# Optimization experiments

Hardware: AMD Instinct MI355X
Metric: run time of the kernel (lower is better)

Reference implementation:

```python
import jax, jax.numpy as jnp
import numpy as np

N = 50000
E = 1600000
DIM = 128
RC = 5.0
DEPTH = 3


def setup_inputs() -> dict:
    key = jax.random.key(0)
    kv, ke, ks, kd, kw, kb, krs, ksig = jax.random.split(key, 8)
    v = jax.random.normal(kv, (N, DIM), dtype=jnp.float32)
    # edge distances in [0, rc]
    e = jax.random.uniform(ke, (E, 1), dtype=jnp.float32) * RC
    src = jax.random.randint(ks, (E,), 0, N, dtype=jnp.int32)
    dst = jax.random.randint(kd, (E,), 0, N, dtype=jnp.int32)
    # learned params: A = nn.Linear(dim, dim); rs, sigma = torch.rand(1)
    A_w = jax.random.normal(kw, (DIM, DIM), dtype=jnp.float32) / np.sqrt(DIM)
    A_b = jax.random.normal(kb, (DIM,), dtype=jnp.float32) * 0.01
    rs = jax.random.uniform(krs, (1,), dtype=jnp.float32)
    sigma = jax.random.uniform(ksig, (1,), dtype=jnp.float32)
    return {"v": v, "e": e, "src": src, "dst": dst,
            "A_w": A_w, "A_b": A_b, "rs": rs, "sigma": sigma}


def _edge_envelope(r, rs, sigma):
    # exp(-(r-rs)^2/sigma^2) * 0.5 * cos(pi*r/rc) * (r < rc)
    gauss = jnp.exp(-jnp.square(r - rs) / jnp.square(sigma))
    cutoff = 0.5 * jnp.cos(np.pi * r / RC) * (r < RC).astype(r.dtype)
    return gauss * cutoff


def reference(v, e, src, dst, A_w, A_b, rs, sigma):
    f = _edge_envelope(e, rs, sigma)  # [E, 1]
    cur = v
    for _ in range(DEPTH):
        msg = f * cur[src]  # gather src node feats, weight by edge envelope: [E, DIM]
        svf = jax.ops.segment_sum(msg, dst, num_segments=N)  # scatter-sum to dst: [N, DIM]
        cur = jax.nn.relu((svf + v) @ A_w.T + A_b)  # linear + relu, skip from original v
    return cur
```

## Files before the change

### kernel.cpp

```cpp
#include <hip/hip_runtime.h>
#include <math.h>

#define N_NODES 50000
#define N_PAD   50048
#define N_EDGES 1600000
#define DIM     128
#define RCUT    5.0f
#define NGROUP  (N_PAD / 64)
#define NB_PRE  512
#define CH_PRE  (N_EDGES / NB_PRE)
#define NB_CONV 6250
#define NB_WPREP 8
#define NB_SUB  8
#define B_SUB   (NB_PRE / NB_SUB)
#define XPAD    136
#define NTILE   (N_PAD / 16)
#define NB_MID  32

typedef __attribute__((ext_vector_type(8))) __bf16 bf16x8;
typedef __attribute__((ext_vector_type(4))) float  f32x4;

__device__ __forceinline__ float bf_lo(unsigned int u) { return __uint_as_float(u << 16); }
__device__ __forceinline__ float bf_hi(unsigned int u) { return __uint_as_float(u & 0xffff0000u); }
__device__ __forceinline__ unsigned short f2bf(float x) {
    unsigned int u = __float_as_uint(x);
    u += 0x7fffu + ((u >> 16) & 1u);
    return (unsigned short)(u >> 16);
}

__global__ __launch_bounds__(256) void preA_kernel(
        const float* __restrict__ v, unsigned short* __restrict__ vb,
        const float* __restrict__ Aw, uint4* __restrict__ wfrag,
        const int* __restrict__ dst, int* __restrict__ partial,
        int* __restrict__ bar) {
    int b = blockIdx.x;
    if (b < NB_CONV) {
        int i = b * 256 + threadIdx.x;
        float4 x = ((const float4*)v)[i];
        uint2 o;
        o.x = (unsigned)f2bf(x.x) | ((unsigned)f2bf(x.y) << 16);
        o.y = (unsigned)f2bf(x.z) | ((unsigned)f2bf(x.w) << 16);
        ((uint2*)vb)[i] = o;
    } else if (b < NB_CONV + NB_WPREP) {
        int t = (b - NB_CONV) * 256 + threadIdx.x;
        if (b == NB_CONV && threadIdx.x <= NB_MID)
            bar[threadIdx.x * 32] = 0;
        int lane = t & 63, nt = (t >> 6) & 7, kk = t >> 9;
        int n  = nt * 16 + (lane & 15);
        int k0 = kk * 32 + (lane >> 4) * 8;
        unsigned short h[8];
        #pragma unroll
        for (int i = 0; i < 8; ++i) h[i] = f2bf(Aw[n * DIM + k0 + i]);
        uint4 o;
        o.x = h[0] | ((unsigned)h[1] << 16); o.y = h[2] | ((unsigned)h[3] << 16);
        o.z = h[4] | ((unsigned)h[5] << 16); o.w = h[6] | ((unsigned)h[7] << 16);
        wfrag[t] = o;
    } else {
        __shared__ int h[NGROUP];
        int cb = b - NB_CONV - NB_WPREP, tid = threadIdx.x;
        for (int g = tid; g < NGROUP; g += 256) h[g] = 0;
        __syncthreads();
        int beg = cb * CH_PRE, end = beg + CH_PRE;
        for (int i = beg + tid; i < end; i += 256)
            atomicAdd(&h[dst[i] >> 6], 1);
        __syncthreads();
        for (int g = tid; g < NGROUP; g += 256) partial[cb * NGROUP + g] = h[g];
    }
}

__device__ __forceinline__ void gsync32(int* bar) {
    int* rel = bar + NB_MID * 32;
    __syncthreads();
    if (threadIdx.x == 0) {
        __threadfence();
        __hip_atomic_store(&bar[blockIdx.x * 32], 1,
                           __ATOMIC_RELAXED, __HIP_MEMORY_SCOPE_AGENT);
    }
    if (blockIdx.x == 0) {
        if (threadIdx.x < NB_MID) {
            int* cp = &bar[threadIdx.x * 32];
            while (__hip_atomic_load(cp, __ATOMIC_RELAXED,
                                     __HIP_MEMORY_SCOPE_AGENT) == 0)
                __builtin_amdgcn_s_sleep(1);
        }
        __syncthreads();
        if (threadIdx.x == 0) {
            __threadfence();
            __hip_atomic_store(rel, 1, __ATOMIC_RELAXED, __HIP_MEMORY_SCOPE_AGENT);
        }
    }
    if (threadIdx.x == 0) {
        while (__hip_atomic_load(rel, __ATOMIC_RELAXED,
                                 __HIP_MEMORY_SCOPE_AGENT) == 0)
            __builtin_amdgcn_s_sleep(1);
        __threadfence();
    }
    __syncthreads();
}

__global__ __launch_bounds__(256) void kmid_kernel(
        const int* __restrict__ partial,
        int* __restrict__ partial2,
        int* __restrict__ goff,
        int* __restrict__ pbase,
        int* __restrict__ bar) {
    __shared__ int part[256];
    __shared__ int goffL[NGROUP];
    int tid = threadIdx.x, bid = blockIdx.x;
    int gb = bid & 3, bb = bid >> 2;
    int g = gb * 256 + tid;

    if (g < NGROUP) {
        int s = 0;
        int b0 = bb * B_SUB;
        for (int b = b0; b < b0 + B_SUB; ++b) s += partial[b * NGROUP + g];
        partial2[bb * NGROUP + g] = s;
    }
    gsync32(bar);

    int i0 = tid * 4;
    int v[4]; int s = 0;
    #pragma unroll
    for (int k = 0; k < 4; ++k) {
        int i = i0 + k; int t = 0;
        if (i < NGROUP) {
            #pragma unroll
            for (int b2 = 0; b2 < NB_SUB; ++b2) t += partial2[b2 * NGROUP + i];
        }
        v[k] = t; s += t;
    }
    part[tid] = s; __syncthreads();
    for (int d = 1; d < 256; d <<= 1) {
        int val = (tid >= d) ? part[tid - d] : 0;
        __syncthreads(); part[tid] += val; __syncthreads();
    }
    int run = (tid == 0) ? 0 : part[tid - 1];
    #pragma unroll
    for (int k = 0; k < 4; ++k) {
        int i = i0 + k;
        if (i < NGROUP) {
            goffL[i] = run;
            if (bid == 0) goff[i] = run;
            run += v[k];
        }
    }
    if (bid == 0 && tid == 0) goff[NGROUP] = N_EDGES;
    __syncthreads();

    if (g < NGROUP) {
        int r = goffL[g];
        for (int b2 = 0; b2 < bb; ++b2) r += partial2[b2 * NGROUP + g];
        int b0 = bb * B_SUB;
        for (int b = b0; b < b0 + B_SUB; ++b) {
            pbase[b * NGROUP + g] = r;
            r += partial[b * NGROUP + g];
        }
    }
}

__global__ __launch_bounds__(512) void reorder_kernel(
        const float* __restrict__ e,
        const int*   __restrict__ src,
        const int*   __restrict__ dst,
        const float* __restrict__ rs,
        const float* __restrict__ sigma,
        const int*   __restrict__ pbase,
        int2* __restrict__ metaT) {
    __shared__ int base[NGROUP];
    __shared__ int cnt[NGROUP];
    int b = blockIdx.x, tid = threadIdx.x;
    for (int g = tid; g < NGROUP; g += 512) { base[g] = pbase[b * NGROUP + g]; cnt[g] = 0; }
    __syncthreads();
    float rsv = rs[0], sg = sigma[0];
    int beg = b * CH_PRE, end = beg + CH_PRE;
    for (int i = beg + tid; i < end; i += 512) {
        float r  = e[i];
        float d  = r - rsv;
        float gauss = expf(-(d * d) / (sg * sg));
        float cut   = 0.5f * cosf(r * (float)(M_PI / (double)RCUT));
        cut = (r < RCUT) ? cut : 0.0f;
        float fe = gauss * cut;
        int dn = dst[i];
        int g  = dn >> 6;
        int lr = atomicAdd(&cnt[g], 1);
        metaT[base[g] + lr] = make_int2(src[i] * (DIM * 2) | ((dn & 63) << 24),
                                        __float_as_int(fe));
    }
}

#define EDGE2(mx, mf, rr)                                        \
    do {                                                         \
        float ff = __int_as_float(mf);                           \
        a0 = fmaf(ff, bf_lo(rr), a0);                            \
        a1 = fmaf(ff, bf_hi(rr), a1);                            \
    } while (0)

__device__ __forceinline__ void gather_node(
        const int2* __restrict__ meta, const char* basec,
        int beg, int end, float& a0, float& a1) {
    int c = beg;
    if ((c & 1) && c < end) {
        int2 m = meta[c];
        unsigned rr = *(const unsigned*)(basec + (unsigned)m.x);
        EDGE2(m.x, m.y, rr);
        ++c;
    }
    for (; c + 16 <= end; c += 16) {
        int4 m0 = *(const int4*)(meta + c);
        int4 m1 = *(const int4*)(meta + c + 2);
        int4 m2 = *(const int4*)(meta + c + 4);
        int4 m3 = *(const int4*)(meta + c + 6);
        int4 m4 = *(const int4*)(meta + c + 8);
        int4 m5 = *(const int4*)(meta + c + 10);
        int4 m6 = *(const int4*)(meta + c + 12);
        int4 m7 = *(const int4*)(meta + c + 14);
        unsigned r0  = *(const unsigned*)(basec + (unsigned)m0.x);
        unsigned r1  = *(const unsigned*)(basec + (unsigned)m0.z);
        unsigned r2  = *(const unsigned*)(basec + (unsigned)m1.x);
        unsigned r3  = *(const unsigned*)(basec + (unsigned)m1.z);
        unsigned r4  = *(const unsigned*)(basec + (unsigned)m2.x);
        unsigned r5  = *(const unsigned*)(basec + (unsigned)m2.z);
        unsigned r6  = *(const unsigned*)(basec + (unsigned)m3.x);
        unsigned r7  = *(const unsigned*)(basec + (unsigned)m3.z);
        unsigned r8  = *(const unsigned*)(basec + (unsigned)m4.x);
        unsigned r9  = *(const unsigned*)(basec + (unsigned)m4.z);
        unsigned r10 = *(const unsigned*)(basec + (unsigned)m5.x);
        unsigned r11 = *(const unsigned*)(basec + (unsigned)m5.z);
        unsigned r12 = *(const unsigned*)(basec + (unsigned)m6.x);
        unsigned r13 = *(const unsigned*)(basec + (unsigned)m6.z);
        unsigned r14 = *(const unsigned*)(basec + (unsigned)m7.x);
        unsigned r15 = *(const unsigned*)(basec + (unsigned)m7.z);
        EDGE2(m0.x, m0.y, r0);  EDGE2(m0.z, m0.w, r1);
        EDGE2(m1.x, m1.y, r2);  EDGE2(m1.z, m1.w, r3);
        EDGE2(m2.x, m2.y, r4);  EDGE2(m2.z, m2.w, r5);
        EDGE2(m3.x, m3.y, r6);  EDGE2(m3.z, m3.w, r7);
        EDGE2(m4.x, m4.y, r8);  EDGE2(m4.z, m4.w, r9);
        EDGE2(m5.x, m5.y, r10); EDGE2(m5.z, m5.w, r11);
        EDGE2(m6.x, m6.y, r12); EDGE2(m6.z, m6.w, r13);
        EDGE2(m7.x, m7.y, r14); EDGE2(m7.z, m7.w, r15);
    }
    if (c + 8 <= end) {
        int4 m0 = *(const int4*)(meta + c);
        int4 m1 = *(const int4*)(meta + c + 2);
        int4 m2 = *(const int4*)(meta + c + 4);
        int4 m3 = *(const int4*)(meta + c + 6);
        unsigned r0 = *(const unsigned*)(basec + (unsigned)m0.x);
        unsigned r1 = *(const unsigned*)(basec + (unsigned)m0.z);
        unsigned r2 = *(const unsigned*)(basec + (unsigned)m1.x);
        unsigned r3 = *(const unsigned*)(basec + (unsigned)m1.z);
        unsigned r4 = *(const unsigned*)(basec + (unsigned)m2.x);
        unsigned r5 = *(const unsigned*)(basec + (unsigned)m2.z);
        unsigned r6 = *(const unsigned*)(basec + (unsigned)m3.x);
        unsigned r7 = *(const unsigned*)(basec + (unsigned)m3.z);
        EDGE2(m0.x, m0.y, r0); EDGE2(m0.z, m0.w, r1);
        EDGE2(m1.x, m1.y, r2); EDGE2(m1.z, m1.w, r3);
        EDGE2(m2.x, m2.y, r4); EDGE2(m2.z, m2.w, r5);
        EDGE2(m3.x, m3.y, r6); EDGE2(m3.z, m3.w, r7);
        c += 8;
    }
    for (; c < end; ++c) {
        int2 m = meta[c];
        unsigned rr = *(const unsigned*)(basec + (unsigned)m.x);
        EDGE2(m.x, m.y, rr);
    }
}

__global__ __launch_bounds__(512) void layer0_kernel(
        const unsigned short* __restrict__ cur,
        const unsigned short* __restrict__ vb,
        const int2*  __restrict__ metaT,
        const int*   __restrict__ goff,
        int2* __restrict__ meta,
        int*  __restrict__ off,
        const uint4* __restrict__ wfrag,
        const float* __restrict__ bias,
        unsigned short* __restrict__ out_bf) {
    __shared__ unsigned short xlds[64 * XPAD];
    __shared__ int c64[64], b64[65], cu64[64];
    int tid = threadIdx.x;
    int wv  = tid >> 6, lane = tid & 63;
    int g   = blockIdx.x;
    int sbeg = goff[g], send = goff[g + 1];

    if (tid < 64) c64[tid] = 0;
    __syncthreads();
    for (int i = sbeg + tid; i < send; i += 512)
        atomicAdd(&c64[(metaT[i].x >> 24) & 63], 1);
    __syncthreads();
    if (tid == 0) {
        int run = 0;
        #pragma unroll
        for (int t = 0; t < 64; ++t) { b64[t] = run; cu64[t] = run; run += c64[t]; }
        b64[64] = run;
    }
    __syncthreads();
    if (tid < 64) {
        int node = g * 64 + tid;
        if (node <= N_NODES) off[node] = sbeg + b64[tid];
    }
    for (int i = sbeg + tid; i < send; i += 512) {
        int2 m = metaT[i];
        int tag = (m.x >> 24) & 63;
        int lr = atomicAdd(&cu64[tag], 1);
        meta[sbeg + lr] = make_int2(m.x & 0x00FFFFFF, m.y);
    }
    __syncthreads();

    int n0 = g * 64 + wv * 8;
    int myoff = 0;
    if (lane < 9) myoff = sbeg + b64[wv * 8 + lane];
    const char* basec = (const char*)cur + lane * 4;

    #pragma unroll 1
    for (int q = 0; q < 8; ++q) {
        int nl = wv * 8 + q;
        int n  = n0 + q;
        float a0 = 0.f, a1 = 0.f;
        if (n < N_NODES) {
            unsigned vv = *(const unsigned*)((const char*)vb + (size_t)n * (DIM * 2) + lane * 4);
            a0 = bf_lo(vv); a1 = bf_hi(vv);
            int beg = __builtin_amdgcn_readlane(myoff, q);
            int end = __builtin_amdgcn_readlane(myoff, q + 1);
            gather_node(meta, basec, beg, end, a0, a1);
        }
        *(unsigned*)(xlds + nl * XPAD + lane * 2) =
            (unsigned)f2bf(a0) | ((unsigned)f2bf(a1) << 16);
    }
    __syncthreads();

    int quad = lane >> 4, l16 = lane & 15;
    int rb = wv >> 1, nh = wv & 1;
    f32x4 acc[4];
    #pragma unroll
    for (int j = 0; j < 4; ++j) acc[j] = (f32x4){0.f, 0.f, 0.f, 0.f};

    const unsigned short* xp = xlds + (rb * 16 + l16) * XPAD + quad * 8;
    #pragma unroll
    for (int kk = 0; kk < 4; ++kk) {
        bf16x8 af = *(const bf16x8*)(xp + kk * 32);
        #pragma unroll
        for (int j = 0; j < 4; ++j) {
            uint4 w = wfrag[(kk * 8 + nh * 4 + j) * 64 + lane];
            bf16x8 bfr = __builtin_bit_cast(bf16x8, w);
            acc[j] = __builtin_amdgcn_mfma_f32_16x16x32_bf16(af, bfr, acc[j], 0, 0, 0);
        }
    }

    int orow0 = g * 64 + rb * 16 + quad * 4;
    #pragma unroll
    for (int j = 0; j < 4; ++j) {
        int col = (nh * 4 + j) * 16 + l16;
        float b = bias[col];
        #pragma unroll
        for (int r = 0; r < 4; ++r) {
            int orow = orow0 + r;
            if (orow < N_NODES)
                out_bf[(size_t)orow * DIM + col] = f2bf(fmaxf(acc[j][r] + b, 0.f));
        }
    }
}

__global__ __launch_bounds__(128, 8) void layer12_kernel(
        const unsigned short* __restrict__ cur,
        const unsigned short* __restrict__ vb,
        const int2*  __restrict__ meta,
        const int*   __restrict__ off,
        const uint4* __restrict__ wfrag,
        const float* __restrict__ bias,
        unsigned short* __restrict__ out_bf,
        float* __restrict__ out_f,
        int last) {
    __shared__ unsigned short xlds[16 * XPAD];
    int tid = threadIdx.x;
    int wv  = tid >> 6, lane = tid & 63;
    int tile = blockIdx.x;
    int n0  = tile * 16 + wv * 8;

    int offidx = n0 + ((lane < 9) ? lane : 8);
    if (offidx > N_NODES) offidx = N_NODES;
    int myoff = off[offidx];
    const char* basec = (const char*)cur + lane * 4;

    #pragma unroll 1
    for (int q = 0; q < 8; ++q) {
        int nl = wv * 8 + q;
        int n  = n0 + q;
        float a0 = 0.f, a1 = 0.f;
        if (n < N_NODES) {
            unsigned vv = *(const unsigned*)((const char*)vb + (size_t)n * (DIM * 2) + lane * 4);
            a0 = bf_lo(vv); a1 = bf_hi(vv);
            int beg = __builtin_amdgcn_readlane(myoff, q);
            int end = __builtin_amdgcn_readlane(myoff, q + 1);
            gather_node(meta, basec, beg, end, a0, a1);
        }
        *(unsigned*)(xlds + nl * XPAD + lane * 2) =
            (unsigned)f2bf(a0) | ((unsigned)f2bf(a1) << 16);
    }
    __syncthreads();

    int quad = lane >> 4, l16 = lane & 15;
    f32x4 acc[4];
    #pragma unroll
    for (int j = 0; j < 4; ++j) acc[j] = (f32x4){0.f, 0.f, 0.f, 0.f};

    const unsigned short* xp = xlds + l16 * XPAD + quad * 8;
    #pragma unroll
    for (int kk = 0; kk < 4; ++kk) {
        bf16x8 af = *(const bf16x8*)(xp + kk * 32);
        #pragma unroll
        for (int j = 0; j < 4; ++j) {
            uint4 w = wfrag[(kk * 8 + wv * 4 + j) * 64 + lane];
            bf16x8 bfr = __builtin_bit_cast(bf16x8, w);
            acc[j] = __builtin_amdgcn_mfma_f32_16x16x32_bf16(af, bfr, acc[j], 0, 0, 0);
        }
    }

    int orow0 = tile * 16 + quad * 4;
    #pragma unroll
    for (int j = 0; j < 4; ++j) {
        int col = (wv * 4 + j) * 16 + l16;
        float b = bias[col];
        #pragma unroll
        for (int r = 0; r < 4; ++r) {
            int orow = orow0 + r;
            if (orow < N_NODES) {
                float val = fmaxf(acc[j][r] + b, 0.f);
                if (last) out_f[(size_t)orow * DIM + col] = val;
                else      out_bf[(size_t)orow * DIM + col] = f2bf(val);
            }
        }
    }
}

extern "C" void kernel_launch(void* const* d_in, const int* in_sizes, int n_in,
                              void* d_out, int out_size, void* d_ws, size_t ws_size,
                              hipStream_t stream) {
    const float* v     = (const float*)d_in[0];
    const float* e     = (const float*)d_in[1];
    const int*   src   = (const int*)  d_in[2];
    const int*   dst   = (const int*)  d_in[3];
    const float* Aw    = (const float*)d_in[4];
    const float* Ab    = (const float*)d_in[5];
    const float* rs    = (const float*)d_in[6];
    const float* sigma = (const float*)d_in[7];
    float* out = (float*)d_out;

    char* p = (char*)d_ws;
    int2*           meta  = (int2*)p;            p += (size_t)N_EDGES * 8;
    unsigned short* bufV  = (unsigned short*)p;  p += (size_t)N_PAD * DIM * 2;
    unsigned short* bufA  = (unsigned short*)p;  p += (size_t)N_PAD * DIM * 2;
    unsigned short* bufB  = (unsigned short*)p;  p += (size_t)N_PAD * DIM * 2;
    uint4*          wfrag = (uint4*)p;           p += 2048 * 16;
    int*            off   = (int*)p;             p += (size_t)(N_NODES + 2) * 4;
    int*            goff  = (int*)p;             p += (NGROUP + 2) * 4;
    int*            bar   = (int*)p;             p += (NB_MID + 1) * 32 * 4;
    int2* metaT    = (int2*)bufA;
    int*  partial  = (int*)bufB;
    int*  pbase    = partial + NB_PRE * NGROUP;
    int*  partial2 = pbase + NB_PRE * NGROUP;

    preA_kernel<<<NB_CONV + NB_WPREP + NB_PRE, 256, 0, stream>>>(
        v, bufV, Aw, wfrag, dst, partial, bar);
    kmid_kernel<<<NB_MID, 256, 0, stream>>>(partial, partial2, goff, pbase, bar);
    reorder_kernel<<<NB_PRE, 512, 0, stream>>>(e, src, dst, rs, sigma, pbase, metaT);

    layer0_kernel<<<NGROUP, 512, 0, stream>>>(
        bufV, bufV, metaT, goff, meta, off, wfrag, Ab, bufB);
    layer12_kernel<<<NTILE, 128, 0, stream>>>(
        bufB, bufV, meta, off, wfrag, Ab, bufA, nullptr, 0);
    layer12_kernel<<<NTILE, 128, 0, stream>>>(
        bufA, bufV, meta, off, wfrag, Ab, nullptr, out, 1);
}
```

Baseline: 318.3 us.

## Bucket edges by 16-node groups and shrink layer0 blocks to 16-node tiles

Changes the counting-sort granularity from 64-node groups to 16-node groups, so the histogram, prefix scan and reorder all work on 3128 buckets. The reorder runs on 128 blocks that each cover four histogram chunks. layer0 now processes one 16-node tile per 128-thread block, matching layer12. This is meant to raise parallelism and occupancy in layer0 and shorten its per-block local sort. In exchange, the mid scan kernel needs more blocks in its grid-wide sync, and the reorder has fewer, larger blocks.

Result: slower. 348.7 us (+9.6%).

```diff
diff --git a/kernel.cpp b/kernel.cpp
--- a/kernel.cpp
+++ b/kernel.cpp
@@ -6,16 +6,16 @@
 #define N_EDGES 1600000
 #define DIM     128
 #define RCUT    5.0f
-#define NGROUP  (N_PAD / 64)
+#define NG16    (N_PAD / 16)
 #define NB_PRE  512
 #define CH_PRE  (N_EDGES / NB_PRE)
 #define NB_CONV 6250
 #define NB_WPREP 8
-#define NB_SUB  8
-#define B_SUB   (NB_PRE / NB_SUB)
+#define NB_RE   128
+#define CH_RE   (N_EDGES / NB_RE)
 #define XPAD    136
-#define NTILE   (N_PAD / 16)
-#define NB_MID  32
+#define NB_MID  104
+#define GCHK    13
 
 typedef __attribute__((ext_vector_type(8))) __bf16 bf16x8;
 typedef __attribute__((ext_vector_type(4))) float  f32x4;
@@ -56,19 +56,19 @@
         o.z = h[4] | ((unsigned)h[5] << 16); o.w = h[6] | ((unsigned)h[7] << 16);
         wfrag[t] = o;
     } else {
-        __shared__ int h[NGROUP];
+        __shared__ int h[NG16];
         int cb = b - NB_CONV - NB_WPREP, tid = threadIdx.x;
-        for (int g = tid; g < NGROUP; g += 256) h[g] = 0;
+        for (int g = tid; g < NG16; g += 256) h[g] = 0;
         __syncthreads();
         int beg = cb * CH_PRE, end = beg + CH_PRE;
         for (int i = beg + tid; i < end; i += 256)
-            atomicAdd(&h[dst[i] >> 6], 1);
+            atomicAdd(&h[dst[i] >> 4], 1);
         __syncthreads();
-        for (int g = tid; g < NGROUP; g += 256) partial[cb * NGROUP + g] = h[g];
-    }
-}
-
-__device__ __forceinline__ void gsync32(int* bar) {
+        for (int g = tid; g < NG16; g += 256) partial[cb * NG16 + g] = h[g];
+    }
+}
+
+__device__ __forceinline__ void gsyncm(int* bar) {
     int* rel = bar + NB_MID * 32;
     __syncthreads();
     if (threadIdx.x == 0) {
@@ -105,29 +105,29 @@
         int* __restrict__ pbase,
         int* __restrict__ bar) {
     __shared__ int part[256];
-    __shared__ int goffL[NGROUP];
+    __shared__ int goffL[NG16];
     int tid = threadIdx.x, bid = blockIdx.x;
-    int gb = bid & 3, bb = bid >> 2;
+    int gb = bid % 13, bb = bid / 13;
     int g = gb * 256 + tid;
 
-    if (g < NGROUP) {
+    if (g < NG16) {
         int s = 0;
-        int b0 = bb * B_SUB;
-        for (int b = b0; b < b0 + B_SUB; ++b) s += partial[b * NGROUP + g];
-        partial2[bb * NGROUP + g] = s;
-    }
-    gsync32(bar);
-
-    int i0 = tid * 4;
-    int v[4]; int s = 0;
-    #pragma unroll
-    for (int k = 0; k < 4; ++k) {
+        int b0 = bb * 64;
+        for (int b = b0; b < b0 + 64; ++b) s += partial[b * NG16 + g];
+        partial2[bb * NG16 + g] = s;
+    }
+    gsyncm(bar);
+
+    int i0 = tid * GCHK;
+    int vv[GCHK]; int s = 0;
+    #pragma unroll
+    for (int k = 0; k < GCHK; ++k) {
         int i = i0 + k; int t = 0;
-        if (i < NGROUP) {
+        if (i < NG16) {
             #pragma unroll
-            for (int b2 = 0; b2 < NB_SUB; ++b2) t += partial2[b2 * NGROUP + i];
-        }
-        v[k] = t; s += t;
+            for (int b2 = 0; b2 < 8; ++b2) t += partial2[b2 * NG16 + i];
+        }
+        vv[k] = t; s += t;
     }
     part[tid] = s; __syncthreads();
     for (int d = 1; d < 256; d <<= 1) {
@@ -136,24 +136,26 @@
     }
     int run = (tid == 0) ? 0 : part[tid - 1];
     #pragma unroll
-    for (int k = 0; k < 4; ++k) {
+    for (int k = 0; k < GCHK; ++k) {
         int i = i0 + k;
-        if (i < NGROUP) {
+        if (i < NG16) {
             goffL[i] = run;
             if (bid == 0) goff[i] = run;
-            run += v[k];
-        }
-    }
-    if (bid == 0 && tid == 0) goff[NGROUP] = N_EDGES;
-    __syncthreads();
-
-    if (g < NGROUP) {
+            run += vv[k];
+        }
+    }
+    if (bid == 0 && tid == 0) goff[NG16] = N_EDGES;
+    __syncthreads();
+
+    if (g < NG16) {
         int r = goffL[g];
-        for (int b2 = 0; b2 < bb; ++b2) r += partial2[b2 * NGROUP + g];
-        int b0 = bb * B_SUB;
-        for (int b = b0; b < b0 + B_SUB; ++b) {
-            pbase[b * NGROUP + g] = r;
-            r += partial[b * NGROUP + g];
+        for (int b2 = 0; b2 < bb; ++b2) r += partial2[b2 * NG16 + g];
+        #pragma unroll 1
+        for (int j = 0; j < 16; ++j) {
+            int rc = bb * 16 + j;
+            pbase[rc * NG16 + g] = r;
+            #pragma unroll
+            for (int c = 0; c < 4; ++c) r += partial[(rc * 4 + c) * NG16 + g];
         }
     }
 }
@@ -166,13 +168,13 @@
         const float* __restrict__ sigma,
         const int*   __restrict__ pbase,
         int2* __restrict__ metaT) {
-    __shared__ int base[NGROUP];
-    __shared__ int cnt[NGROUP];
+    __shared__ int base[NG16];
+    __shared__ int cnt[NG16];
     int b = blockIdx.x, tid = threadIdx.x;
-    for (int g = tid; g < NGROUP; g += 512) { base[g] = pbase[b * NGROUP + g]; cnt[g] = 0; }
+    for (int g = tid; g < NG16; g += 512) { base[g] = pbase[b * NG16 + g]; cnt[g] = 0; }
     __syncthreads();
     float rsv = rs[0], sg = sigma[0];
-    int beg = b * CH_PRE, end = beg + CH_PRE;
+    int beg = b * CH_RE, end = beg + CH_RE;
     for (int i = beg + tid; i < end; i += 512) {
         float r  = e[i];
         float d  = r - rsv;
@@ -181,9 +183,9 @@
         cut = (r < RCUT) ? cut : 0.0f;
         float fe = gauss * cut;
         int dn = dst[i];
-        int g  = dn >> 6;
+        int g  = dn >> 4;
         int lr = atomicAdd(&cnt[g], 1);
-        metaT[base[g] + lr] = make_int2(src[i] * (DIM * 2) | ((dn & 63) << 24),
+        metaT[base[g] + lr] = make_int2(src[i] * (DIM * 2) | ((dn & 15) << 24),
                                         __float_as_int(fe));
     }
 }
@@ -265,7 +267,7 @@
     }
 }
 
-__global__ __launch_bounds__(512) void layer0_kernel(
+__global__ __launch_bounds__(128, 8) void layer0_kernel(
         const unsigned short* __restrict__ cur,
         const unsigned short* __restrict__ vb,
         const int2*  __restrict__ metaT,
@@ -275,40 +277,40 @@
         const uint4* __restrict__ wfrag,
         const float* __restrict__ bias,
         unsigned short* __restrict__ out_bf) {
-    __shared__ unsigned short xlds[64 * XPAD];
-    __shared__ int c64[64], b64[65], cu64[64];
+    __shared__ unsigned short xlds[16 * XPAD];
+    __shared__ int c16[16], b16[17], cu16[16];
     int tid = threadIdx.x;
     int wv  = tid >> 6, lane = tid & 63;
-    int g   = blockIdx.x;
-    int sbeg = goff[g], send = goff[g + 1];
-
-    if (tid < 64) c64[tid] = 0;
-    __syncthreads();
-    for (int i = sbeg + tid; i < send; i += 512)
-        atomicAdd(&c64[(metaT[i].x >> 24) & 63], 1);
+    int t   = blockIdx.x;
+    int sbeg = goff[t], send = goff[t + 1];
+
+    if (tid < 16) c16[tid] = 0;
+    __syncthreads();
+    for (int i = sbeg + tid; i < send; i += 128)
+        atomicAdd(&c16[(metaT[i].x >> 24) & 15], 1);
     __syncthreads();
     if (tid == 0) {
         int run = 0;
         #pragma unroll
-        for (int t = 0; t < 64; ++t) { b64[t] = run; cu64[t] = run; run += c64[t]; }
-        b64[64] = run;
-    }
-    __syncthreads();
-    if (tid < 64) {
-        int node = g * 64 + tid;
-        if (node <= N_NODES) off[node] = sbeg + b64[tid];
-    }
-    for (int i = sbeg + tid; i < send; i += 512) {
+        for (int k = 0; k < 16; ++k) { b16[k] = run; cu16[k] = run; run += c16[k]; }
+        b16[16] = run;
+    }
+    __syncthreads();
+    if (tid < 17) {
+        int node = t * 16 + tid;
+        if (node <= N_NODES) off[node] = sbeg + b16[tid];
+    }
+    for (int i = sbeg + tid; i < send; i += 128) {
         int2 m = metaT[i];
-        int tag = (m.x >> 24) & 63;
-        int lr = atomicAdd(&cu64[tag], 1);
+        int tag = (m.x >> 24) & 15;
+        int lr = atomicAdd(&cu16[tag], 1);
         meta[sbeg + lr] = make_int2(m.x & 0x00FFFFFF, m.y);
     }
     __syncthreads();
 
-    int n0 = g * 64 + wv * 8;
+    int n0 = t * 16 + wv * 8;
     int myoff = 0;
-    if (lane < 9) myoff = sbeg + b64[wv * 8 + lane];
+    if (lane < 9) myoff = sbeg + b16[wv * 8 + lane];
     const char* basec = (const char*)cur + lane * 4;
 
     #pragma unroll 1
@@ -329,27 +331,26 @@
     __syncthreads();
 
     int quad = lane >> 4, l16 = lane & 15;
-    int rb = wv >> 1, nh = wv & 1;
     f32x4 acc[4];
     #pragma unroll
     for (int j = 0; j < 4; ++j) acc[j] = (f32x4){0.f, 0.f, 0.f, 0.f};
 
-    const unsigned short* xp = xlds + (rb * 16 + l16) * XPAD + quad * 8;
+    const unsigned short* xp = xlds + l16 * XPAD + quad * 8;
     #pragma unroll
     for (int kk = 0; kk < 4; ++kk) {
         bf16x8 af = *(const bf16x8*)(xp + kk * 32);
         #pragma unroll
         for (int j = 0; j < 4; ++j) {
-            uint4 w = wfrag[(kk * 8 + nh * 4 + j) * 64 + lane];
+            uint4 w = wfrag[(kk * 8 + wv * 4 + j) * 64 + lane];
             bf16x8 bfr = __builtin_bit_cast(bf16x8, w);
             acc[j] = __builtin_amdgcn_mfma_f32_16x16x32_bf16(af, bfr, acc[j], 0, 0, 0);
         }
     }
 
-    int orow0 = g * 64 + rb * 16 + quad * 4;
+    int orow0 = t * 16 + quad * 4;
     #pragma unroll
     for (int j = 0; j < 4; ++j) {
-        int col = (nh * 4 + j) * 16 + l16;
+        int col = (wv * 4 + j) * 16 + l16;
         float b = bias[col];
         #pragma unroll
         for (int r = 0; r < 4; ++r) {
@@ -452,22 +453,22 @@
     unsigned short* bufB  = (unsigned short*)p;  p += (size_t)N_PAD * DIM * 2;
     uint4*          wfrag = (uint4*)p;           p += 2048 * 16;
     int*            off   = (int*)p;             p += (size_t)(N_NODES + 2) * 4;
-    int*            goff  = (int*)p;             p += (NGROUP + 2) * 4;
+    int*            goff  = (int*)p;             p += (NG16 + 2) * 4;
     int*            bar   = (int*)p;             p += (NB_MID + 1) * 32 * 4;
     int2* metaT    = (int2*)bufA;
     int*  partial  = (int*)bufB;
-    int*  pbase    = partial + NB_PRE * NGROUP;
-    int*  partial2 = pbase + NB_PRE * NGROUP;
+    int*  pbase    = partial + NB_PRE * NG16;
+    int*  partial2 = pbase + NB_RE * NG16;
 
     preA_kernel<<<NB_CONV + NB_WPREP + NB_PRE, 256, 0, stream>>>(
         v, bufV, Aw, wfrag, dst, partial, bar);
     kmid_kernel<<<NB_MID, 256, 0, stream>>>(partial, partial2, goff, pbase, bar);
-    reorder_kernel<<<NB_PRE, 512, 0, stream>>>(e, src, dst, rs, sigma, pbase, metaT);
-
-    layer0_kernel<<<NGROUP, 512, 0, stream>>>(
+    reorder_kernel<<<NB_RE, 512, 0, stream>>>(e, src, dst, rs, sigma, pbase, metaT);
+
+    layer0_kernel<<<NG16, 128, 0, stream>>>(
         bufV, bufV, metaT, goff, meta, off, wfrag, Ab, bufB);
-    layer12_kernel<<<NTILE, 128, 0, stream>>>(
+    layer12_kernel<<<NG16, 128, 0, stream>>>(
         bufB, bufV, meta, off, wfrag, Ab, bufA, nullptr, 0);
-    layer12_kernel<<<NTILE, 128, 0, stream>>>(
+    layer12_kernel<<<NG16, 128, 0, stream>>>(
         bufA, bufV, meta, off, wfrag, Ab, nullptr, out, 1);
 }
```
